# Optimization experiments

Hardware: AMD Instinct MI355X
Metric: run time of the kernel (lower is better)

Reference implementation:

```python
import jax, jax.numpy as jnp
import numpy as np

NUM_HEADS = 8
EPS = 1e-12  # torch F.normalize eps


def _l2norm(x, axis):
    n = jnp.sqrt(jnp.sum(x * x, axis=axis, keepdims=True))
    return x / jnp.maximum(n, EPS)


def setup_inputs() -> dict:
    key = jax.random.key(0)
    ks = jax.random.split(key, 8)
    n, h, w, dim = 4, 48, 48, 256
    x0 = jax.random.normal(ks[0], (n, h, w, dim), jnp.float32)
    x1 = jax.random.normal(ks[1], (n, h, w, dim), jnp.float32)
    mask = jnp.ones((n, h, w), dtype=bool)
    s = 1.0 / np.sqrt(dim)
    W0 = jax.random.normal(ks[2], (dim, dim), jnp.float32) * s
    b0 = jnp.zeros((dim,), jnp.float32)
    W1 = jax.random.normal(ks[3], (dim, 2 * dim), jnp.float32) * s
    b1 = jnp.zeros((2 * dim,), jnp.float32)
    Wo = jax.random.normal(ks[4], (dim, dim), jnp.float32) * s
    bo = jnp.zeros((dim,), jnp.float32)
    alpha = jnp.ones((1,), jnp.float32)
    beta = jnp.zeros((1,), jnp.float32)
    return {"x0": x0, "x1": x1, "mask": mask, "W0": W0, "b0": b0,
            "W1": W1, "b1": b1, "Wo": Wo, "bo": bo,
            "alpha": alpha, "beta": beta}


def reference(x0, x1, mask, W0, b0, W1, b1, Wo, bo, alpha, beta):
    n, h, w, dim = x0.shape
    heads = NUM_HEADS
    hd = dim // heads
    L = h * w
    # proj0 -> queries: (n, heads, L, hd)
    p0 = (x0.reshape(n, L, dim) @ W0 + b0).reshape(n, L, heads, hd)
    p0 = jnp.transpose(p0, (0, 2, 1, 3))
    # proj1 -> keys/values: channel split of each head's 2*hd block
    pv = (x1.reshape(n, L, dim) @ W1 + b1).reshape(n, L, heads, 2 * hd)
    pv = jnp.transpose(pv, (0, 2, 1, 3))  # (n, heads, L, 2*hd)
    p1, v1 = pv[..., :hd], pv[..., hd:]
    # cosine similarity over head_dim
    p0 = _l2norm(p0, axis=-1)
    p1 = _l2norm(p1, axis=-1)
    sim = jnp.einsum('nhqd,nhkd->nhqk', p0, p1)  # (n, heads, L, L)
    sim = alpha * sim + beta
    sim = jnp.where(mask.reshape(n, 1, 1, L), sim, -jnp.inf)
    sim = jax.nn.sigmoid(sim)
    max_sim = jnp.max(sim, axis=-1)      # (n, heads, L)
    idx = jnp.argmax(sim, axis=-1)       # (n, heads, L)
    gathered = jnp.take_along_axis(v1, idx[..., None], axis=2)  # (n, heads, L, hd)
    message = max_sim[..., None] * gathered
    message = jnp.transpose(message, (0, 2, 1, 3)).reshape(n, h, w, dim)
    return message @ Wo + bo
```

## Files before the change

kernel.cpp:

```cpp
#include <hip/hip_runtime.h>
#include <math.h>

#define NB      4
#define LL      2304
#define DIM     256
#define NHEADS  8
#define HD      32
#define NPAIR   32
#define MM      9216
#define NTILE   144
#define KCHUNK  256
#define NCHUNKS 9
#define CAP     16

typedef __attribute__((ext_vector_type(8))) short bf16x8;
typedef __attribute__((ext_vector_type(4))) float f32x4;

__device__ __forceinline__ unsigned short f2bf(float x) {
    unsigned u = __float_as_uint(x);
    u = u + 0x7FFF + ((u >> 16) & 1);
    return (unsigned short)(u >> 16);
}

__device__ __forceinline__ void gload_lds16(const void* g, void* l) {
    __builtin_amdgcn_global_load_lds(
        (const __attribute__((address_space(1))) void*)g,
        (__attribute__((address_space(3))) void*)l, 16, 0, 0);
}

template<int N, int KLOC>
__device__ __forceinline__ void gemm_tile_64x64(
    const float* __restrict__ A, const float* __restrict__ W,
    int m0, int n0, int kbase, int tid, float acc[4][4],
    float As[32][68], float Ws[32][64])
{
    const int tx = tid & 15, ty = tid >> 4;
    const int wv = __builtin_amdgcn_readfirstlane(tid >> 6);
    for (int k0 = 0; k0 < KLOC; k0 += 32) {
        __syncthreads();
        #pragma unroll
        for (int i = 0; i < 2; ++i) {
            int e4 = tid + i * 256;
            int kr = e4 >> 4, nc = (e4 & 15) * 4;
            gload_lds16(&W[(size_t)(kbase + k0 + kr) * N + n0 + nc],
                        &Ws[0][0] + (size_t)(wv * 64 + i * 256) * 4);
        }
        #pragma unroll
        for (int i = 0; i < 2; ++i) {
            int e4 = tid + i * 256;
            int m  = e4 >> 3;
            int kk = (e4 & 7) * 4;
            float4 v = *(const float4*)&A[(size_t)(m0 + m) * DIM + kbase + k0 + kk];
            As[kk + 0][m] = v.x;
            As[kk + 1][m] = v.y;
            As[kk + 2][m] = v.z;
            As[kk + 3][m] = v.w;
        }
        __syncthreads();
        #pragma unroll 8
        for (int d = 0; d < 32; ++d) {
            float4 a4 = *(const float4*)&As[d][ty * 4];
            float4 b4 = *(const float4*)&Ws[d][tx * 4];
            float av[4] = {a4.x, a4.y, a4.z, a4.w};
            float bv[4] = {b4.x, b4.y, b4.z, b4.w};
            #pragma unroll
            for (int qi = 0; qi < 4; ++qi)
                #pragma unroll
                for (int ki = 0; ki < 4; ++ki)
                    acc[qi][ki] = fmaf(av[qi], bv[ki], acc[qi][ki]);
        }
    }
}

__global__ __launch_bounds__(256) void proj_fused_kernel(
    const float* __restrict__ x0, const float* __restrict__ W0,
    const float* __restrict__ b0,
    const float* __restrict__ x1, const float* __restrict__ W1,
    const float* __restrict__ b1,
    float* __restrict__ p0r, unsigned short* __restrict__ p0b,
    float* __restrict__ p1r, unsigned short* __restrict__ p1b,
    float* __restrict__ v1)
{
    __shared__ float As[32][68];
    __shared__ float Ws[32][64];
    const int tid = threadIdx.x;
    const int tx = tid & 15, ty = tid >> 4;
    const int by = blockIdx.y;
    const int m0 = blockIdx.x * 64;

    float acc[4][4] = {};

    if (by < 4) {
        const int n0 = by * 64;
        gemm_tile_64x64<DIM, DIM>(x0, W0, m0, n0, 0, tid, acc, As, Ws);
        float4 bb = *(const float4*)&b0[n0 + tx * 4];
        float bv[4] = {bb.x, bb.y, bb.z, bb.w};
        const int h  = 2 * by + (tx >> 3);
        const int d0 = (tx & 7) * 4;
        #pragma unroll
        for (int qi = 0; qi < 4; ++qi) {
            float c0 = acc[qi][0] + bv[0];
            float c1 = acc[qi][1] + bv[1];
            float c2 = acc[qi][2] + bv[2];
            float c3 = acc[qi][3] + bv[3];
            float ss = c0 * c0 + c1 * c1 + c2 * c2 + c3 * c3;
            ss += __shfl_xor(ss, 1);
            ss += __shfl_xor(ss, 2);
            ss += __shfl_xor(ss, 4);
            float sc = 1.0f / fmaxf(sqrtf(ss), 1e-12f);
            int m = m0 + ty * 4 + qi;
            int n_idx = m / LL, l = m - n_idx * LL;
            size_t rb = ((size_t)(n_idx * NHEADS + h) * LL + l) * HD + d0;
            float4 o = {c0 * sc, c1 * sc, c2 * sc, c3 * sc};
            *(float4*)&p0r[rb] = o;
            *(ushort4*)&p0b[rb] = make_ushort4(f2bf(o.x), f2bf(o.y),
                                               f2bf(o.z), f2bf(o.w));
        }
    } else {
        const int h = by - 4;
        const int n0 = h * 64;
        gemm_tile_64x64<2 * DIM, DIM>(x1, W1, m0, n0, 0, tid, acc, As, Ws);
        float4 bb = *(const float4*)&b1[n0 + tx * 4];
        float bv[4] = {bb.x, bb.y, bb.z, bb.w};
        #pragma unroll
        for (int qi = 0; qi < 4; ++qi) {
            float c0 = acc[qi][0] + bv[0];
            float c1 = acc[qi][1] + bv[1];
            float c2 = acc[qi][2] + bv[2];
            float c3 = acc[qi][3] + bv[3];
            float ss = c0 * c0 + c1 * c1 + c2 * c2 + c3 * c3;
            ss += __shfl_xor(ss, 1);
            ss += __shfl_xor(ss, 2);
            ss += __shfl_xor(ss, 4);
            float sc = 1.0f / fmaxf(sqrtf(ss), 1e-12f);
            int m = m0 + ty * 4 + qi;
            int n_idx = m / LL, l = m - n_idx * LL;
            size_t row = (size_t)(n_idx * NHEADS + h) * LL + l;
            if (tx < 8) {
                size_t rb = row * HD + tx * 4;
                float4 o = {c0 * sc, c1 * sc, c2 * sc, c3 * sc};
                *(float4*)&p1r[rb] = o;
                *(ushort4*)&p1b[rb] = make_ushort4(f2bf(o.x), f2bf(o.y),
                                                   f2bf(o.z), f2bf(o.w));
            } else {
                float4 o = {c0, c1, c2, c3};
                *(float4*)&v1[row * HD + (tx - 8) * 4] = o;
            }
        }
    }
}

__device__ __forceinline__ void rescue(const float* __restrict__ q,
                                       const float* __restrict__ k,
                                       float a, float b, int kidx,
                                       float& bv, int& bi) {
    float dot = 0.f;
    #pragma unroll
    for (int j = 0; j < 8; ++j) {
        float4 qq = *(const float4*)&q[j * 4];
        float4 kk = *(const float4*)&k[j * 4];
        dot = fmaf(qq.x, kk.x, dot);
        dot = fmaf(qq.y, kk.y, dot);
        dot = fmaf(qq.z, kk.z, dot);
        dot = fmaf(qq.w, kk.w, dot);
    }
    float te = fmaf(a, dot, b);
    if (te > bv || (te == bv && kidx < bi)) { bv = te; bi = kidx; }
}

__global__ __launch_bounds__(256) void sim_fused_kernel(
    const unsigned short* __restrict__ p0b,
    const unsigned short* __restrict__ p1b,
    const float* __restrict__ p0r, const float* __restrict__ p1r,
    const float* __restrict__ v1,
    const float* __restrict__ alpha, const float* __restrict__ beta,
    float* __restrict__ msg)
{
    __shared__ __align__(16) unsigned short Bs[2][KCHUNK * HD];
    __shared__ unsigned int   s_cnt[128];
    __shared__ unsigned short s_list[128 * CAP];

    const int tid = threadIdx.x;
    const int w = tid >> 6, l = tid & 63;
    const int wu = __builtin_amdgcn_readfirstlane(w);
    const int col = l & 15, quad = l >> 4;
    const int lin  = blockIdx.x;
    const int xcd  = lin & 7;
    const int slot = lin >> 3;
    const int pair = ((slot & 3) << 3) | xcd;
    const int rb_blk = (slot >> 2) * 128;
    const int rowbase = rb_blk + w * 32;
    const float a = alpha[0], b = beta[0];
    const float margin = (a == 0.f) ? INFINITY : (2.5f * 0.00395f + 1e-5f);
    const bool neg = (a < 0.f);

    if (tid < 128) s_cnt[tid] = 0;

    bf16x8 af[2];
    #pragma unroll
    for (int g = 0; g < 2; ++g) {
        af[g] = *(const bf16x8*)
            (p0b + ((size_t)pair * LL + rowbase + g * 16 + col) * HD + quad * 8);
        if (neg) {
            #pragma unroll
            for (int e = 0; e < 8; ++e) af[g][e] ^= (short)0x8000;
        }
    }

    const char* Bg = (const char*)(p1b + (size_t)pair * LL * HD);
    const int srcperm = (l & 15) * 64 + (l >> 4) * 16;

    auto STAGE = [&](int c, int buf) {
        #pragma unroll
        for (int i = 0; i < 4; ++i) {
            const int t = i * 4 + wu;
            gload_lds16(Bg + (size_t)c * 16384 + t * 1024 + srcperm,
                        (char*)&Bs[buf][0] + t * 1024);
        }
    };

    float mx[2][4];
    #pragma unroll
    for (int g = 0; g < 2; ++g)
        #pragma unroll
        for (int r = 0; r < 4; ++r) mx[g][r] = -INFINITY;

    STAGE(0, 0);
    __syncthreads();
    for (int c = 0; c < NCHUNKS; ++c) {
        const int cur = c & 1;
        if (c + 1 < NCHUNKS) STAGE(c + 1, cur ^ 1);
        const char* bb = (const char*)&Bs[cur][0];
        #pragma unroll
        for (int t8 = 0; t8 < 16; ++t8) {
            bf16x8 bf = *(const bf16x8*)(bb + t8 * 1024 + l * 16);
            #pragma unroll
            for (int g = 0; g < 2; ++g) {
                f32x4 cc = __builtin_amdgcn_mfma_f32_16x16x32_bf16(
                    af[g], bf, (f32x4){0.f, 0.f, 0.f, 0.f}, 0, 0, 0);
                #pragma unroll
                for (int r = 0; r < 4; ++r)
                    mx[g][r] = fmaxf(mx[g][r], cc[r]);
            }
        }
        __syncthreads();
    }

    #pragma unroll
    for (int mask = 1; mask <= 8; mask <<= 1)
        #pragma unroll
        for (int g = 0; g < 2; ++g)
            #pragma unroll
            for (int r = 0; r < 4; ++r)
                mx[g][r] = fmaxf(mx[g][r], __shfl_xor(mx[g][r], mask));
    float thr[2][4];
    #pragma unroll
    for (int g = 0; g < 2; ++g)
        #pragma unroll
        for (int r = 0; r < 4; ++r) thr[g][r] = mx[g][r] - margin;

    STAGE(0, 0);
    __syncthreads();
    for (int c = 0; c < NCHUNKS; ++c) {
        const int cur = c & 1;
        if (c + 1 < NCHUNKS) STAGE(c + 1, cur ^ 1);
        const char* bb = (const char*)&Bs[cur][0];
        #pragma unroll
        for (int t8 = 0; t8 < 16; ++t8) {
            bf16x8 bf = *(const bf16x8*)(bb + t8 * 1024 + l * 16);
            f32x4 cc[2];
            #pragma unroll
            for (int g = 0; g < 2; ++g)
                cc[g] = __builtin_amdgcn_mfma_f32_16x16x32_bf16(
                    af[g], bf, (f32x4){0.f, 0.f, 0.f, 0.f}, 0, 0, 0);
            bool any = false;
            bool fl[2][4];
            #pragma unroll
            for (int g = 0; g < 2; ++g)
                #pragma unroll
                for (int r = 0; r < 4; ++r) {
                    fl[g][r] = cc[g][r] >= thr[g][r];
                    any = any | fl[g][r];
                }
            if (any) {
                int k = c * KCHUNK + t8 * 16 + col;
                #pragma unroll
                for (int g = 0; g < 2; ++g)
                    #pragma unroll
                    for (int r = 0; r < 4; ++r)
                        if (fl[g][r]) {
                            int row = w * 32 + g * 16 + quad * 4 + r;
                            unsigned s = atomicAdd(&s_cnt[row], 1u);
                            if (s < CAP)
                                s_list[row * CAP + s] = (unsigned short)k;
                        }
            }
        }
        __syncthreads();
    }

    if (tid < 128) {
        const int row = rb_blk + tid;
        const float* qr = p0r + ((size_t)pair * LL + row) * HD;
        const float* pk = p1r + (size_t)pair * LL * HD;
        float bv = -INFINITY;
        int   bi = 0x7FFFFFFF;
        unsigned n = s_cnt[tid];
        if (n > CAP) {
            for (int k = 0; k < LL; ++k)
                rescue(qr, pk + (size_t)k * HD, a, b, k, bv, bi);
        } else {
            for (unsigned s = 0; s < n; ++s) {
                int k = s_list[tid * CAP + s];
                rescue(qr, pk + (size_t)k * HD, a, b, k, bv, bi);
            }
        }
        const int n_idx = pair >> 3, h = pair & 7;
        float ms = 1.0f / (1.0f + __expf(-bv));
        const float* vsrc = &v1[((size_t)pair * LL + bi) * HD];
        float* mdst = &msg[((size_t)n_idx * LL + row) * DIM + h * HD];
        #pragma unroll
        for (int j = 0; j < 8; ++j) {
            float4 vv = *(const float4*)&vsrc[j * 4];
            float4 o = {ms * vv.x, ms * vv.y, ms * vv.z, ms * vv.w};
            *(float4*)&mdst[j * 4] = o;
        }
    }
}

__global__ __launch_bounds__(256) void out_gemm_kernel(
    const float* __restrict__ A, const float* __restrict__ W,
    const float* __restrict__ bo, float* __restrict__ out)
{
    __shared__ float As[32][68];
    __shared__ float Ws[32][64];
    const int tid = threadIdx.x;
    const int tx = tid & 15, ty = tid >> 4;
    const int m0 = blockIdx.x * 64, n0 = blockIdx.y * 64;

    float acc[4][4] = {};
    gemm_tile_64x64<DIM, DIM>(A, W, m0, n0, 0, tid, acc, As, Ws);

    float4 bb = *(const float4*)&bo[n0 + tx * 4];
    #pragma unroll
    for (int qi = 0; qi < 4; ++qi) {
        int m = m0 + ty * 4 + qi;
        float4 o = {acc[qi][0] + bb.x, acc[qi][1] + bb.y,
                    acc[qi][2] + bb.z, acc[qi][3] + bb.w};
        *(float4*)&out[(size_t)m * DIM + n0 + tx * 4] = o;
    }
}

extern "C" void kernel_launch(void* const* d_in, const int* in_sizes, int n_in,
                              void* d_out, int out_size, void* d_ws, size_t ws_size,
                              hipStream_t stream) {
    const float* x0    = (const float*)d_in[0];
    const float* x1    = (const float*)d_in[1];
    const float* W0    = (const float*)d_in[3];
    const float* b0    = (const float*)d_in[4];
    const float* W1    = (const float*)d_in[5];
    const float* b1    = (const float*)d_in[6];
    const float* Wo    = (const float*)d_in[7];
    const float* bo    = (const float*)d_in[8];
    const float* alpha = (const float*)d_in[9];
    const float* beta  = (const float*)d_in[10];
    float* out = (float*)d_out;

    const size_t E = (size_t)NPAIR * LL * HD;
    float* ws     = (float*)d_ws;
    float* p0r    = ws;
    float* p1r    = p0r + E;
    float* v1     = p1r + E;
    float* msg    = v1 + E;
    float* rowmax = msg + (size_t)MM * DIM;
    unsigned short* p0b = (unsigned short*)(rowmax + (size_t)NPAIR * LL);
    unsigned short* p1b = p0b + E;

    proj_fused_kernel<<<dim3(MM / 64, 12), 256, 0, stream>>>(
        x0, W0, b0, x1, W1, b1, p0r, p0b, p1r, p1b, v1);
    sim_fused_kernel<<<dim3(576), 256, 0, stream>>>(
        p0b, p1b, p0r, p1r, v1, alpha, beta, msg);
    out_gemm_kernel<<<dim3(MM / 64, DIM / 64), 256, 0, stream>>>(
        msg, Wo, bo, out);
}
```

Measured before the change: 222.3 us.

## Halve rows per block in sim kernel, double grid, prefetch B fragments

Each block of the fused similarity/argmax kernel now covers 64 query rows instead of 128. Each wave handles 16 rows with a single MFMA A fragment, and the grid doubles to 1152 blocks. The inner loops also keep four LDS B fragments in flight as a rolling prefetch. The aim is more parallelism and occupancy across the CUs and hiding LDS read latency. The cost is that each block now stages the full key set for half as many rows, which doubles global/L2 traffic for p1b and the per-row key reuse drops.

```diff
diff --git a/kernel.cpp b/kernel.cpp
--- a/kernel.cpp
+++ b/kernel.cpp
@@ -177,8 +177,8 @@
     float* __restrict__ msg)
 {
     __shared__ __align__(16) unsigned short Bs[2][KCHUNK * HD];
-    __shared__ unsigned int   s_cnt[128];
-    __shared__ unsigned short s_list[128 * CAP];
+    __shared__ unsigned int   s_cnt[64];
+    __shared__ unsigned short s_list[64 * CAP];
 
     const int tid = threadIdx.x;
     const int w = tid >> 6, l = tid & 63;
@@ -188,23 +188,19 @@
     const int xcd  = lin & 7;
     const int slot = lin >> 3;
     const int pair = ((slot & 3) << 3) | xcd;
-    const int rb_blk = (slot >> 2) * 128;
-    const int rowbase = rb_blk + w * 32;
+    const int rb_blk = (slot >> 2) * 64;
+    const int rowbase = rb_blk + w * 16;
     const float a = alpha[0], b = beta[0];
     const float margin = (a == 0.f) ? INFINITY : (2.5f * 0.00395f + 1e-5f);
     const bool neg = (a < 0.f);
 
-    if (tid < 128) s_cnt[tid] = 0;
-
-    bf16x8 af[2];
-    #pragma unroll
-    for (int g = 0; g < 2; ++g) {
-        af[g] = *(const bf16x8*)
-            (p0b + ((size_t)pair * LL + rowbase + g * 16 + col) * HD + quad * 8);
-        if (neg) {
-            #pragma unroll
-            for (int e = 0; e < 8; ++e) af[g][e] ^= (short)0x8000;
-        }
+    if (tid < 64) s_cnt[tid] = 0;
+
+    bf16x8 af = *(const bf16x8*)
+        (p0b + ((size_t)pair * LL + rowbase + col) * HD + quad * 8);
+    if (neg) {
+        #pragma unroll
+        for (int e = 0; e < 8; ++e) af[e] ^= (short)0x8000;
     }
 
     const char* Bg = (const char*)(p1b + (size_t)pair * LL * HD);
@@ -219,11 +215,7 @@
         }
     };
 
-    float mx[2][4];
-    #pragma unroll
-    for (int g = 0; g < 2; ++g)
-        #pragma unroll
-        for (int r = 0; r < 4; ++r) mx[g][r] = -INFINITY;
+    float mx[4] = {-INFINITY, -INFINITY, -INFINITY, -INFINITY};
 
     STAGE(0, 0);
     __syncthreads();
@@ -231,17 +223,20 @@
         const int cur = c & 1;
         if (c + 1 < NCHUNKS) STAGE(c + 1, cur ^ 1);
         const char* bb = (const char*)&Bs[cur][0];
-        #pragma unroll
-        for (int t8 = 0; t8 < 16; ++t8) {
-            bf16x8 bf = *(const bf16x8*)(bb + t8 * 1024 + l * 16);
+        bf16x8 pf[4];
+        #pragma unroll
+        for (int u = 0; u < 4; ++u)
+            pf[u] = *(const bf16x8*)(bb + u * 1024 + l * 16);
+        #pragma unroll
+        for (int t = 0; t < 16; ++t) {
+            bf16x8 bf = pf[t & 3];
+            if (t + 4 < 16)
+                pf[t & 3] = *(const bf16x8*)(bb + (t + 4) * 1024 + l * 16);
+            f32x4 cc = __builtin_amdgcn_mfma_f32_16x16x32_bf16(
+                af, bf, (f32x4){0.f, 0.f, 0.f, 0.f}, 0, 0, 0);
             #pragma unroll
-            for (int g = 0; g < 2; ++g) {
-                f32x4 cc = __builtin_amdgcn_mfma_f32_16x16x32_bf16(
-                    af[g], bf, (f32x4){0.f, 0.f, 0.f, 0.f}, 0, 0, 0);
-                #pragma unroll
-                for (int r = 0; r < 4; ++r)
-                    mx[g][r] = fmaxf(mx[g][r], cc[r]);
-            }
+            for (int r = 0; r < 4; ++r)
+                mx[r] = fmaxf(mx[r], cc[r]);
         }
         __syncthreads();
     }
@@ -249,15 +244,11 @@
     #pragma unroll
     for (int mask = 1; mask <= 8; mask <<= 1)
         #pragma unroll
-        for (int g = 0; g < 2; ++g)
-            #pragma unroll
-            for (int r = 0; r < 4; ++r)
-                mx[g][r] = fmaxf(mx[g][r], __shfl_xor(mx[g][r], mask));
-    float thr[2][4];
+        for (int r = 0; r < 4; ++r)
+            mx[r] = fmaxf(mx[r], __shfl_xor(mx[r], mask));
+    float thr[4];
     #pragma unroll
-    for (int g = 0; g < 2; ++g)
-        #pragma unroll
-        for (int r = 0; r < 4; ++r) thr[g][r] = mx[g][r] - margin;
+    for (int r = 0; r < 4; ++r) thr[r] = mx[r] - margin;
 
     STAGE(0, 0);
     __syncthreads();
@@ -265,41 +256,37 @@
         const int cur = c & 1;
         if (c + 1 < NCHUNKS) STAGE(c + 1, cur ^ 1);
         const char* bb = (const char*)&Bs[cur][0];
-        #pragma unroll
-        for (int t8 = 0; t8 < 16; ++t8) {
-            bf16x8 bf = *(const bf16x8*)(bb + t8 * 1024 + l * 16);
-            f32x4 cc[2];
-            #pragma unroll
-            for (int g = 0; g < 2; ++g)
-                cc[g] = __builtin_amdgcn_mfma_f32_16x16x32_bf16(
-                    af[g], bf, (f32x4){0.f, 0.f, 0.f, 0.f}, 0, 0, 0);
-            bool any = false;
-            bool fl[2][4];
-            #pragma unroll
-            for (int g = 0; g < 2; ++g)
+        bf16x8 pf[4];
+        #pragma unroll
+        for (int u = 0; u < 4; ++u)
+            pf[u] = *(const bf16x8*)(bb + u * 1024 + l * 16);
+        #pragma unroll
+        for (int t = 0; t < 16; ++t) {
+            bf16x8 bf = pf[t & 3];
+            if (t + 4 < 16)
+                pf[t & 3] = *(const bf16x8*)(bb + (t + 4) * 1024 + l * 16);
+            f32x4 cc = __builtin_amdgcn_mfma_f32_16x16x32_bf16(
+                af, bf, (f32x4){0.f, 0.f, 0.f, 0.f}, 0, 0, 0);
+            bool f0 = cc[0] >= thr[0], f1 = cc[1] >= thr[1];
+            bool f2 = cc[2] >= thr[2], f3 = cc[3] >= thr[3];
+            if (f0 | f1 | f2 | f3) {
+                int k = c * KCHUNK + t * 16 + col;
                 #pragma unroll
                 for (int r = 0; r < 4; ++r) {
-                    fl[g][r] = cc[g][r] >= thr[g][r];
-                    any = any | fl[g][r];
+                    bool fr = (r == 0) ? f0 : (r == 1) ? f1 : (r == 2) ? f2 : f3;
+                    if (fr) {
+                        int row = w * 16 + quad * 4 + r;
+                        unsigned s = atomicAdd(&s_cnt[row], 1u);
+                        if (s < CAP)
+                            s_list[row * CAP + s] = (unsigned short)k;
+                    }
                 }
-            if (any) {
-                int k = c * KCHUNK + t8 * 16 + col;
-                #pragma unroll
-                for (int g = 0; g < 2; ++g)
-                    #pragma unroll
-                    for (int r = 0; r < 4; ++r)
-                        if (fl[g][r]) {
-                            int row = w * 32 + g * 16 + quad * 4 + r;
-                            unsigned s = atomicAdd(&s_cnt[row], 1u);
-                            if (s < CAP)
-                                s_list[row * CAP + s] = (unsigned short)k;
-                        }
             }
         }
         __syncthreads();
     }
 
-    if (tid < 128) {
+    if (tid < 64) {
         const int row = rb_blk + tid;
         const float* qr = p0r + ((size_t)pair * LL + row) * HD;
         const float* pk = p1r + (size_t)pair * LL * HD;
@@ -378,7 +365,7 @@
 
     proj_fused_kernel<<<dim3(MM / 64, 12), 256, 0, stream>>>(
         x0, W0, b0, x1, W1, b1, p0r, p0b, p1r, p1b, v1);
-    sim_fused_kernel<<<dim3(576), 256, 0, stream>>>(
+    sim_fused_kernel<<<dim3(1152), 256, 0, stream>>>(
         p0b, p1b, p0r, p1r, v1, alpha, beta, msg);
     out_gemm_kernel<<<dim3(MM / 64, DIM / 64), 256, 0, stream>>>(
         msg, Wo, bo, out);
```

Result: slower. 230.3 us (+3.6%).

## Move projection and output GEMMs to bf16 MFMA with split-precision emulation

Applied to the files above, without the earlier changes.

Replaces the scalar FP32 LDS-tiled GEMMs for the input projections and the output projection with bf16 MFMA kernels. FP32 accuracy is emulated by splitting operands into hi/mid/lo bf16 parts (6 MFMAs per tile for the projections, 2 for the output). A new prep kernel transposes and splits the weights every call, and the message buffer is now written as bf16 to halve its traffic. Operands are loaded straight from global memory without LDS staging, which may cost bandwidth and adds a fourth launch. Storing messages in bf16 also reduces output precision.

```diff
diff --git a/kernel.cpp b/kernel.cpp
--- a/kernel.cpp
+++ b/kernel.cpp
@@ -8,7 +8,6 @@
 #define HD      32
 #define NPAIR   32
 #define MM      9216
-#define NTILE   144
 #define KCHUNK  256
 #define NCHUNKS 9
 #define CAP     16
@@ -28,123 +27,191 @@
         (__attribute__((address_space(3))) void*)l, 16, 0, 0);
 }
 
-template<int N, int KLOC>
-__device__ __forceinline__ void gemm_tile_64x64(
-    const float* __restrict__ A, const float* __restrict__ W,
-    int m0, int n0, int kbase, int tid, float acc[4][4],
-    float As[32][68], float Ws[32][64])
+__device__ __forceinline__ f32x4 mfma_bb(bf16x8 a, bf16x8 b, f32x4 c) {
+    return __builtin_amdgcn_mfma_f32_16x16x32_bf16(a, b, c, 0, 0, 0);
+}
+
+__device__ __forceinline__ void split8_3(const float* __restrict__ p,
+                                         bf16x8& hi, bf16x8& mid, bf16x8& lo) {
+    float4 u = *(const float4*)p;
+    float4 v = *(const float4*)(p + 4);
+    float xs[8] = {u.x, u.y, u.z, u.w, v.x, v.y, v.z, v.w};
+    #pragma unroll
+    for (int i = 0; i < 8; ++i) {
+        unsigned short h = f2bf(xs[i]);
+        float hf = __uint_as_float((unsigned)h << 16);
+        float r1 = xs[i] - hf;
+        unsigned short m = f2bf(r1);
+        float mf = __uint_as_float((unsigned)m << 16);
+        hi[i]  = (short)h;
+        mid[i] = (short)m;
+        lo[i]  = (short)f2bf(r1 - mf);
+    }
+}
+
+__global__ __launch_bounds__(256) void prep_wt_kernel(
+    const float* __restrict__ W0, const float* __restrict__ W1,
+    const float* __restrict__ Wo,
+    unsigned short* __restrict__ W0t_h, unsigned short* __restrict__ W0t_m,
+    unsigned short* __restrict__ W0t_l,
+    unsigned short* __restrict__ W1t_h, unsigned short* __restrict__ W1t_m,
+    unsigned short* __restrict__ W1t_l,
+    unsigned short* __restrict__ Wot_h, unsigned short* __restrict__ Wot_l)
 {
-    const int tx = tid & 15, ty = tid >> 4;
-    const int wv = __builtin_amdgcn_readfirstlane(tid >> 6);
-    for (int k0 = 0; k0 < KLOC; k0 += 32) {
-        __syncthreads();
-        #pragma unroll
-        for (int i = 0; i < 2; ++i) {
-            int e4 = tid + i * 256;
-            int kr = e4 >> 4, nc = (e4 & 15) * 4;
-            gload_lds16(&W[(size_t)(kbase + k0 + kr) * N + n0 + nc],
-                        &Ws[0][0] + (size_t)(wv * 64 + i * 256) * 4);
-        }
-        #pragma unroll
-        for (int i = 0; i < 2; ++i) {
-            int e4 = tid + i * 256;
-            int m  = e4 >> 3;
-            int kk = (e4 & 7) * 4;
-            float4 v = *(const float4*)&A[(size_t)(m0 + m) * DIM + kbase + k0 + kk];
-            As[kk + 0][m] = v.x;
-            As[kk + 1][m] = v.y;
-            As[kk + 2][m] = v.z;
-            As[kk + 3][m] = v.w;
-        }
-        __syncthreads();
-        #pragma unroll 8
-        for (int d = 0; d < 32; ++d) {
-            float4 a4 = *(const float4*)&As[d][ty * 4];
-            float4 b4 = *(const float4*)&Ws[d][tx * 4];
-            float av[4] = {a4.x, a4.y, a4.z, a4.w};
-            float bv[4] = {b4.x, b4.y, b4.z, b4.w};
-            #pragma unroll
-            for (int qi = 0; qi < 4; ++qi)
-                #pragma unroll
-                for (int ki = 0; ki < 4; ++ki)
-                    acc[qi][ki] = fmaf(av[qi], bv[ki], acc[qi][ki]);
-        }
-    }
-}
-
-__global__ __launch_bounds__(256) void proj_fused_kernel(
-    const float* __restrict__ x0, const float* __restrict__ W0,
-    const float* __restrict__ b0,
-    const float* __restrict__ x1, const float* __restrict__ W1,
-    const float* __restrict__ b1,
+    int idx = blockIdx.x * 256 + threadIdx.x;
+    if (idx < 65536) {
+        int n = idx >> 8, k = idx & 255;
+        float v = W0[k * 256 + n];
+        unsigned short h = f2bf(v);
+        float hf = __uint_as_float((unsigned)h << 16);
+        float r1 = v - hf;
+        unsigned short m = f2bf(r1);
+        float mf = __uint_as_float((unsigned)m << 16);
+        W0t_h[idx] = h; W0t_m[idx] = m; W0t_l[idx] = f2bf(r1 - mf);
+    } else if (idx < 196608) {
+        int j = idx - 65536; int n = j >> 8, k = j & 255;
+        float v = W1[k * 512 + n];
+        unsigned short h = f2bf(v);
+        float hf = __uint_as_float((unsigned)h << 16);
+        float r1 = v - hf;
+        unsigned short m = f2bf(r1);
+        float mf = __uint_as_float((unsigned)m << 16);
+        W1t_h[j] = h; W1t_m[j] = m; W1t_l[j] = f2bf(r1 - mf);
+    } else {
+        int j = idx - 196608; int n = j >> 8, k = j & 255;
+        float v = Wo[k * 256 + n];
+        unsigned short h = f2bf(v);
+        float hf = __uint_as_float((unsigned)h << 16);
+        Wot_h[j] = h; Wot_l[j] = f2bf(v - hf);
+    }
+}
+
+__global__ __launch_bounds__(256) void proj_mfma_kernel(
+    const float* __restrict__ x0, const float* __restrict__ x1,
+    const unsigned short* __restrict__ W0t_h, const unsigned short* __restrict__ W0t_m,
+    const unsigned short* __restrict__ W0t_l,
+    const unsigned short* __restrict__ W1t_h, const unsigned short* __restrict__ W1t_m,
+    const unsigned short* __restrict__ W1t_l,
+    const float* __restrict__ b0, const float* __restrict__ b1,
     float* __restrict__ p0r, unsigned short* __restrict__ p0b,
     float* __restrict__ p1r, unsigned short* __restrict__ p1b,
     float* __restrict__ v1)
 {
-    __shared__ float As[32][68];
-    __shared__ float Ws[32][64];
     const int tid = threadIdx.x;
-    const int tx = tid & 15, ty = tid >> 4;
+    const int w = tid >> 6, l = tid & 63;
+    const int col = l & 15, quad = l >> 4;
     const int by = blockIdx.y;
-    const int m0 = blockIdx.x * 64;
-
-    float acc[4][4] = {};
+    const int m0 = blockIdx.x * 128;
+    const int rowbase = m0 + w * 32;
+
+    const float* A;
+    const unsigned short *Bh, *Bm, *Bl;
+    int nc0;
+    if (by < 4) { A = x0; Bh = W0t_h; Bm = W0t_m; Bl = W0t_l; nc0 = by * 64; }
+    else        { A = x1; Bh = W1t_h; Bm = W1t_m; Bl = W1t_l; nc0 = (by - 4) * 64; }
+
+    f32x4 acc[2][4];
+    #pragma unroll
+    for (int g = 0; g < 2; ++g)
+        #pragma unroll
+        for (int s = 0; s < 4; ++s) acc[g][s] = (f32x4){0.f, 0.f, 0.f, 0.f};
+
+    #pragma unroll
+    for (int kk = 0; kk < DIM; kk += 32) {
+        bf16x8 ah[2], am[2], al[2];
+        #pragma unroll
+        for (int g = 0; g < 2; ++g)
+            split8_3(&A[(size_t)(rowbase + g * 16 + col) * DIM + kk + quad * 8],
+                     ah[g], am[g], al[g]);
+        #pragma unroll
+        for (int s = 0; s < 4; ++s) {
+            size_t boff = (size_t)(nc0 + s * 16 + col) * DIM + kk + quad * 8;
+            bf16x8 bh = *(const bf16x8*)&Bh[boff];
+            bf16x8 bm = *(const bf16x8*)&Bm[boff];
+            bf16x8 bl = *(const bf16x8*)&Bl[boff];
+            #pragma unroll
+            for (int g = 0; g < 2; ++g) {
+                acc[g][s] = mfma_bb(ah[g], bh, acc[g][s]);
+                acc[g][s] = mfma_bb(ah[g], bm, acc[g][s]);
+                acc[g][s] = mfma_bb(am[g], bh, acc[g][s]);
+                acc[g][s] = mfma_bb(am[g], bm, acc[g][s]);
+                acc[g][s] = mfma_bb(ah[g], bl, acc[g][s]);
+                acc[g][s] = mfma_bb(al[g], bh, acc[g][s]);
+            }
+        }
+    }
+
+    const int n_idx = m0 / LL;
+    const int lbase = rowbase - n_idx * LL + quad * 4;
 
     if (by < 4) {
-        const int n0 = by * 64;
-        gemm_tile_64x64<DIM, DIM>(x0, W0, m0, n0, 0, tid, acc, As, Ws);
-        float4 bb = *(const float4*)&b0[n0 + tx * 4];
-        float bv[4] = {bb.x, bb.y, bb.z, bb.w};
-        const int h  = 2 * by + (tx >> 3);
-        const int d0 = (tx & 7) * 4;
-        #pragma unroll
-        for (int qi = 0; qi < 4; ++qi) {
-            float c0 = acc[qi][0] + bv[0];
-            float c1 = acc[qi][1] + bv[1];
-            float c2 = acc[qi][2] + bv[2];
-            float c3 = acc[qi][3] + bv[3];
-            float ss = c0 * c0 + c1 * c1 + c2 * c2 + c3 * c3;
-            ss += __shfl_xor(ss, 1);
-            ss += __shfl_xor(ss, 2);
-            ss += __shfl_xor(ss, 4);
-            float sc = 1.0f / fmaxf(sqrtf(ss), 1e-12f);
-            int m = m0 + ty * 4 + qi;
-            int n_idx = m / LL, l = m - n_idx * LL;
-            size_t rb = ((size_t)(n_idx * NHEADS + h) * LL + l) * HD + d0;
-            float4 o = {c0 * sc, c1 * sc, c2 * sc, c3 * sc};
-            *(float4*)&p0r[rb] = o;
-            *(ushort4*)&p0b[rb] = make_ushort4(f2bf(o.x), f2bf(o.y),
-                                               f2bf(o.z), f2bf(o.w));
+        const int hbase = by * 2;
+        #pragma unroll
+        for (int g = 0; g < 2; ++g) {
+            #pragma unroll
+            for (int pp = 0; pp < 2; ++pp) {
+                f32x4 e0 = acc[g][2 * pp], e1 = acc[g][2 * pp + 1];
+                float bias0 = b0[nc0 + pp * 32 + col];
+                float bias1 = b0[nc0 + pp * 32 + 16 + col];
+                f32x4 ss;
+                #pragma unroll
+                for (int r = 0; r < 4; ++r) {
+                    e0[r] += bias0; e1[r] += bias1;
+                    ss[r] = e0[r] * e0[r] + e1[r] * e1[r];
+                }
+                #pragma unroll
+                for (int mask = 1; mask <= 8; mask <<= 1)
+                    #pragma unroll
+                    for (int r = 0; r < 4; ++r)
+                        ss[r] += __shfl_xor(ss[r], mask);
+                const int pair = n_idx * NHEADS + hbase + pp;
+                #pragma unroll
+                for (int r = 0; r < 4; ++r) {
+                    float sc = 1.0f / fmaxf(sqrtf(ss[r]), 1e-12f);
+                    float a0 = e0[r] * sc, a1 = e1[r] * sc;
+                    size_t base = ((size_t)pair * LL + lbase + g * 16 + r) * HD;
+                    p0r[base + col]      = a0;
+                    p0r[base + 16 + col] = a1;
+                    p0b[base + col]      = f2bf(a0);
+                    p0b[base + 16 + col] = f2bf(a1);
+                }
+            }
         }
     } else {
         const int h = by - 4;
-        const int n0 = h * 64;
-        gemm_tile_64x64<2 * DIM, DIM>(x1, W1, m0, n0, 0, tid, acc, As, Ws);
-        float4 bb = *(const float4*)&b1[n0 + tx * 4];
-        float bv[4] = {bb.x, bb.y, bb.z, bb.w};
-        #pragma unroll
-        for (int qi = 0; qi < 4; ++qi) {
-            float c0 = acc[qi][0] + bv[0];
-            float c1 = acc[qi][1] + bv[1];
-            float c2 = acc[qi][2] + bv[2];
-            float c3 = acc[qi][3] + bv[3];
-            float ss = c0 * c0 + c1 * c1 + c2 * c2 + c3 * c3;
-            ss += __shfl_xor(ss, 1);
-            ss += __shfl_xor(ss, 2);
-            ss += __shfl_xor(ss, 4);
-            float sc = 1.0f / fmaxf(sqrtf(ss), 1e-12f);
-            int m = m0 + ty * 4 + qi;
-            int n_idx = m / LL, l = m - n_idx * LL;
-            size_t row = (size_t)(n_idx * NHEADS + h) * LL + l;
-            if (tx < 8) {
-                size_t rb = row * HD + tx * 4;
-                float4 o = {c0 * sc, c1 * sc, c2 * sc, c3 * sc};
-                *(float4*)&p1r[rb] = o;
-                *(ushort4*)&p1b[rb] = make_ushort4(f2bf(o.x), f2bf(o.y),
-                                                   f2bf(o.z), f2bf(o.w));
-            } else {
-                float4 o = {c0, c1, c2, c3};
-                *(float4*)&v1[row * HD + (tx - 8) * 4] = o;
+        const int pair = n_idx * NHEADS + h;
+        float bias0 = b1[nc0 + col],      bias1 = b1[nc0 + 16 + col];
+        float bias2 = b1[nc0 + 32 + col], bias3 = b1[nc0 + 48 + col];
+        #pragma unroll
+        for (int g = 0; g < 2; ++g) {
+            f32x4 e0 = acc[g][0], e1 = acc[g][1];
+            f32x4 ss;
+            #pragma unroll
+            for (int r = 0; r < 4; ++r) {
+                e0[r] += bias0; e1[r] += bias1;
+                ss[r] = e0[r] * e0[r] + e1[r] * e1[r];
+            }
+            #pragma unroll
+            for (int mask = 1; mask <= 8; mask <<= 1)
+                #pragma unroll
+                for (int r = 0; r < 4; ++r)
+                    ss[r] += __shfl_xor(ss[r], mask);
+            #pragma unroll
+            for (int r = 0; r < 4; ++r) {
+                float sc = 1.0f / fmaxf(sqrtf(ss[r]), 1e-12f);
+                float a0 = e0[r] * sc, a1 = e1[r] * sc;
+                size_t base = ((size_t)pair * LL + lbase + g * 16 + r) * HD;
+                p1r[base + col]      = a0;
+                p1r[base + 16 + col] = a1;
+                p1b[base + col]      = f2bf(a0);
+                p1b[base + 16 + col] = f2bf(a1);
+            }
+            f32x4 e2 = acc[g][2], e3 = acc[g][3];
+            #pragma unroll
+            for (int r = 0; r < 4; ++r) {
+                size_t base = ((size_t)pair * LL + lbase + g * 16 + r) * HD;
+                v1[base + col]      = e2[r] + bias2;
+                v1[base + 16 + col] = e3[r] + bias3;
             }
         }
     }
@@ -174,7 +241,7 @@
     const float* __restrict__ p0r, const float* __restrict__ p1r,
     const float* __restrict__ v1,
     const float* __restrict__ alpha, const float* __restrict__ beta,
-    float* __restrict__ msg)
+    unsigned short* __restrict__ msgh)
 {
     __shared__ __align__(16) unsigned short Bs[2][KCHUNK * HD];
     __shared__ unsigned int   s_cnt[128];
@@ -318,36 +385,65 @@
         const int n_idx = pair >> 3, h = pair & 7;
         float ms = 1.0f / (1.0f + __expf(-bv));
         const float* vsrc = &v1[((size_t)pair * LL + bi) * HD];
-        float* mdst = &msg[((size_t)n_idx * LL + row) * DIM + h * HD];
+        size_t mbase = ((size_t)n_idx * LL + row) * DIM + h * HD;
         #pragma unroll
         for (int j = 0; j < 8; ++j) {
             float4 vv = *(const float4*)&vsrc[j * 4];
-            float4 o = {ms * vv.x, ms * vv.y, ms * vv.z, ms * vv.w};
-            *(float4*)&mdst[j * 4] = o;
-        }
-    }
-}
-
-__global__ __launch_bounds__(256) void out_gemm_kernel(
-    const float* __restrict__ A, const float* __restrict__ W,
+            *(ushort4*)&msgh[mbase + j * 4] = make_ushort4(
+                f2bf(ms * vv.x), f2bf(ms * vv.y),
+                f2bf(ms * vv.z), f2bf(ms * vv.w));
+        }
+    }
+}
+
+__global__ __launch_bounds__(256) void out_mfma_kernel(
+    const unsigned short* __restrict__ msgh,
+    const unsigned short* __restrict__ Wot_h, const unsigned short* __restrict__ Wot_l,
     const float* __restrict__ bo, float* __restrict__ out)
 {
-    __shared__ float As[32][68];
-    __shared__ float Ws[32][64];
     const int tid = threadIdx.x;
-    const int tx = tid & 15, ty = tid >> 4;
-    const int m0 = blockIdx.x * 64, n0 = blockIdx.y * 64;
-
-    float acc[4][4] = {};
-    gemm_tile_64x64<DIM, DIM>(A, W, m0, n0, 0, tid, acc, As, Ws);
-
-    float4 bb = *(const float4*)&bo[n0 + tx * 4];
-    #pragma unroll
-    for (int qi = 0; qi < 4; ++qi) {
-        int m = m0 + ty * 4 + qi;
-        float4 o = {acc[qi][0] + bb.x, acc[qi][1] + bb.y,
-                    acc[qi][2] + bb.z, acc[qi][3] + bb.w};
-        *(float4*)&out[(size_t)m * DIM + n0 + tx * 4] = o;
+    const int w = tid >> 6, l = tid & 63;
+    const int col = l & 15, quad = l >> 4;
+    const int n0 = blockIdx.y * 64;
+    const int m0 = blockIdx.x * 128;
+    const int rowbase = m0 + w * 32;
+
+    f32x4 acc[2][4];
+    #pragma unroll
+    for (int g = 0; g < 2; ++g)
+        #pragma unroll
+        for (int s = 0; s < 4; ++s) acc[g][s] = (f32x4){0.f, 0.f, 0.f, 0.f};
+
+    #pragma unroll
+    for (int kk = 0; kk < DIM; kk += 32) {
+        bf16x8 ah[2];
+        #pragma unroll
+        for (int g = 0; g < 2; ++g)
+            ah[g] = *(const bf16x8*)
+                &msgh[(size_t)(rowbase + g * 16 + col) * DIM + kk + quad * 8];
+        #pragma unroll
+        for (int s = 0; s < 4; ++s) {
+            size_t boff = (size_t)(n0 + s * 16 + col) * DIM + kk + quad * 8;
+            bf16x8 bh = *(const bf16x8*)&Wot_h[boff];
+            bf16x8 bl = *(const bf16x8*)&Wot_l[boff];
+            #pragma unroll
+            for (int g = 0; g < 2; ++g) {
+                acc[g][s] = mfma_bb(ah[g], bh, acc[g][s]);
+                acc[g][s] = mfma_bb(ah[g], bl, acc[g][s]);
+            }
+        }
+    }
+
+    #pragma unroll
+    for (int s = 0; s < 4; ++s) {
+        float bb = bo[n0 + s * 16 + col];
+        #pragma unroll
+        for (int g = 0; g < 2; ++g)
+            #pragma unroll
+            for (int r = 0; r < 4; ++r) {
+                int m = rowbase + g * 16 + quad * 4 + r;
+                out[(size_t)m * DIM + n0 + s * 16 + col] = acc[g][s][r] + bb;
+            }
     }
 }
 
@@ -367,19 +463,29 @@
     float* out = (float*)d_out;
 
     const size_t E = (size_t)NPAIR * LL * HD;
-    float* ws     = (float*)d_ws;
-    float* p0r    = ws;
-    float* p1r    = p0r + E;
-    float* v1     = p1r + E;
-    float* msg    = v1 + E;
-    float* rowmax = msg + (size_t)MM * DIM;
-    unsigned short* p0b = (unsigned short*)(rowmax + (size_t)NPAIR * LL);
-    unsigned short* p1b = p0b + E;
-
-    proj_fused_kernel<<<dim3(MM / 64, 12), 256, 0, stream>>>(
-        x0, W0, b0, x1, W1, b1, p0r, p0b, p1r, p1b, v1);
+    float* ws  = (float*)d_ws;
+    float* p0r = ws;
+    float* p1r = p0r + E;
+    float* v1  = p1r + E;
+    unsigned short* p0b   = (unsigned short*)(v1 + E);
+    unsigned short* p1b   = p0b + E;
+    unsigned short* msgh  = p1b + E;
+    unsigned short* W0t_h = msgh + E;
+    unsigned short* W0t_m = W0t_h + 65536;
+    unsigned short* W0t_l = W0t_m + 65536;
+    unsigned short* W1t_h = W0t_l + 65536;
+    unsigned short* W1t_m = W1t_h + 131072;
+    unsigned short* W1t_l = W1t_m + 131072;
+    unsigned short* Wot_h = W1t_l + 131072;
+    unsigned short* Wot_l = Wot_h + 65536;
+
+    prep_wt_kernel<<<1024, 256, 0, stream>>>(
+        W0, W1, Wo, W0t_h, W0t_m, W0t_l, W1t_h, W1t_m, W1t_l, Wot_h, Wot_l);
+    proj_mfma_kernel<<<dim3(MM / 128, 12), 256, 0, stream>>>(
+        x0, x1, W0t_h, W0t_m, W0t_l, W1t_h, W1t_m, W1t_l, b0, b1,
+        p0r, p0b, p1r, p1b, v1);
     sim_fused_kernel<<<dim3(576), 256, 0, stream>>>(
-        p0b, p1b, p0r, p1r, v1, alpha, beta, msg);
-    out_gemm_kernel<<<dim3(MM / 64, DIM / 64), 256, 0, stream>>>(
-        msg, Wo, bo, out);
-}
+        p0b, p1b, p0r, p1r, v1, alpha, beta, msgh);
+    out_mfma_kernel<<<dim3(MM / 128, 4), 256, 0, stream>>>(
+        msgh, Wot_h, Wot_l, bo, out);
+}
```

New measurement: 238.1 us. +7.1%, slower.
